# Optimization experiments

Measured on AMD Instinct MI355X. Metric: run time of the kernel, lower is better.

Reference implementation:

```python
import jax, jax.numpy as jnp
import numpy as np

B, C, H, W = 4, 96, 256, 256
WS = 8          # window size
NH = 4          # num heads
SHIFT = 4       # shift size (block_idx=1 -> WS//2)
HD = C // NH    # head dim = 24
N = WS * WS     # tokens per window = 64
MLP_H = 4 * C   # 384
EPS = 1e-6


def _rel_pos_index():
    coords = np.stack(np.meshgrid(np.arange(WS), np.arange(WS), indexing='ij'))  # [2,WS,WS]
    cf = coords.reshape(2, -1)                                                   # [2,N]
    rel = cf[:, :, None] - cf[:, None, :]                                        # [2,N,N]
    rel = rel.transpose(1, 2, 0) + (WS - 1)
    rel[:, :, 0] *= 2 * WS - 1
    return rel.sum(-1)  # [N,N] int


def _attn_mask():
    # standard Swin shifted-window mask, static (numpy)
    img = np.zeros((H, W), dtype=np.float32)
    cnt = 0
    for hs in (slice(0, -WS), slice(-WS, -SHIFT), slice(-SHIFT, None)):
        for ws_ in (slice(0, -WS), slice(-WS, -SHIFT), slice(-SHIFT, None)):
            img[hs, ws_] = cnt
            cnt += 1
    m = img.reshape(H // WS, WS, W // WS, WS).transpose(0, 2, 1, 3).reshape(-1, N)  # [nW,N]
    am = m[:, None, :] - m[:, :, None]
    return np.where(am != 0, -100.0, 0.0).astype(np.float32)  # [nW,N,N]


REL_IDX = _rel_pos_index()
ATTN_MASK = _attn_mask()


def _ln(x, w, b):
    mu = x.mean(-1, keepdims=True)
    var = ((x - mu) ** 2).mean(-1, keepdims=True)
    return (x - mu) * jax.lax.rsqrt(var + EPS) * w + b


def setup_inputs() -> dict:
    key = jax.random.key(0)
    ks = jax.random.split(key, 8)
    s = 0.02
    return {
        'x': jax.random.normal(ks[0], (B, C, H, W), jnp.float32),
        'norm_w': jnp.ones((C,), jnp.float32),
        'norm_b': jnp.zeros((C,), jnp.float32),
        'qkv_w': jax.random.normal(ks[1], (3 * C, C), jnp.float32) * s,
        'qkv_b': jnp.zeros((3 * C,), jnp.float32),
        'proj_w': jax.random.normal(ks[2], (C, C), jnp.float32) * s,
        'proj_b': jnp.zeros((C,), jnp.float32),
        'rpb_table': jax.random.normal(ks[3], ((2 * WS - 1) ** 2, NH), jnp.float32) * s,
        'norm2_w': jnp.ones((C,), jnp.float32),
        'norm2_b': jnp.zeros((C,), jnp.float32),
        'fc1_w': jax.random.normal(ks[4], (MLP_H, C), jnp.float32) * s,
        'fc1_b': jnp.zeros((MLP_H,), jnp.float32),
        'fc2_w': jax.random.normal(ks[5], (C, MLP_H), jnp.float32) * s,
        'fc2_b': jnp.zeros((C,), jnp.float32),
    }


def _swin_msa(y, qkv_w, qkv_b, proj_w, proj_b, rpb_table):
    # y: [B,H,W,C] (already layer-normed)
    ys = jnp.roll(y, shift=(-SHIFT, -SHIFT), axis=(1, 2))
    nWh, nWw = H // WS, W // WS
    # window partition -> [B*nW, N, C]
    xw = ys.reshape(B, nWh, WS, nWw, WS, C).transpose(0, 1, 3, 2, 4, 5).reshape(-1, N, C)
    qkv = xw @ qkv_w.T + qkv_b                       # [Bn,N,3C]
    qkv = qkv.reshape(-1, N, 3, NH, HD).transpose(2, 0, 3, 1, 4)  # [3,Bn,NH,N,HD]
    q, k, v = qkv[0], qkv[1], qkv[2]
    scale = HD ** -0.5
    attn = jnp.einsum('bhnd,bhmd->bhnm', q * scale, k)           # [Bn,NH,N,N]
    bias = rpb_table[jnp.asarray(REL_IDX)].transpose(2, 0, 1)    # [NH,N,N]
    attn = attn + bias[None]
    nW = nWh * nWw
    mask = jnp.asarray(ATTN_MASK)                                # [nW,N,N]
    attn = attn.reshape(B, nW, NH, N, N) + mask[None, :, None]
    attn = jax.nn.softmax(attn.reshape(-1, NH, N, N), axis=-1)
    out = jnp.einsum('bhnm,bhmd->bhnd', attn, v)                 # [Bn,NH,N,HD]
    out = out.transpose(0, 2, 1, 3).reshape(-1, N, C)
    out = out @ proj_w.T + proj_b
    # window reverse
    out = out.reshape(B, nWh, nWw, WS, WS, C).transpose(0, 1, 3, 2, 4, 5).reshape(B, H, W, C)
    return jnp.roll(out, shift=(SHIFT, SHIFT), axis=(1, 2))


def reference(x, norm_w, norm_b, qkv_w, qkv_b, proj_w, proj_b, rpb_table,
              norm2_w, norm2_b, fc1_w, fc1_b, fc2_w, fc2_b):
    xp = x.transpose(0, 2, 3, 1)                                  # [B,H,W,C]
    h = xp + _swin_msa(_ln(xp, norm_w, norm_b), qkv_w, qkv_b, proj_w, proj_b, rpb_table)
    y2 = _ln(h, norm2_w, norm2_b)
    mlp = jax.nn.gelu(y2 @ fc1_w.T + fc1_b, approximate=False) @ fc2_w.T + fc2_b
    h = h + mlp                                                   # proj is Identity (in==out)
    return h.transpose(0, 3, 1, 2)
```

## Files before the change

### kernel.cpp

```cpp
#include <hip/hip_runtime.h>
#include <hip/hip_bf16.h>
#include <math.h>

constexpr int B_    = 4;
constexpr int C_    = 96;
constexpr int H_    = 256;
constexpr int W_    = 256;
constexpr int WS_   = 8;
constexpr int NH_   = 4;
constexpr int SHIFT_= 4;
constexpr int HD_   = 24;
constexpr int NT_   = 64;
constexpr int NWW_  = 32;
constexpr int MLPH_ = 384;
constexpr int HW_   = H_*W_;
constexpr float EPS_   = 1e-6f;
constexpr float SCALE_ = 0.20412414523193150f;

using bf16   = __bf16;
using bf16x8 = __attribute__((ext_vector_type(8))) __bf16;
using bf16x4 = __attribute__((ext_vector_type(4))) __bf16;
using f32x4  = __attribute__((ext_vector_type(4))) float;

__device__ __forceinline__ f32x4 mfma16(bf16x8 a, bf16x8 b, f32x4 c) {
    return __builtin_amdgcn_mfma_f32_16x16x32_bf16(a, b, c, 0, 0, 0);
}

constexpr size_t XT_B    = (size_t)B_*HW_*96*2;
constexpr int    WQ2_E   = 320*96;
constexpr int    WPR_E   = 96*96;
constexpr int    WF1_E   = 384*96;
constexpr int    WF2_E   = 96*384;
constexpr int    WSUM_E  = WQ2_E + WPR_E + WF1_E + WF2_E;
constexpr int    NBQ     = 320;
constexpr int    WBLKS   = (WSUM_E + NBQ + 255)/256;
constexpr int    TBLKS   = B_*HW_/64;

__global__ __launch_bounds__(256) void prep_kernel(
    const float* __restrict__ x,
    const float* __restrict__ qkv_w, const float* __restrict__ qkv_b,
    const float* __restrict__ proj_w, const float* __restrict__ fc1w,
    const float* __restrict__ fc2w,
    bf16* __restrict__ xt, bf16* __restrict__ warena, float* __restrict__ bq2)
{
    __shared__ float st[64*97];
    const int tid = threadIdx.x;
    if (blockIdx.x < WBLKS) {
        int i = blockIdx.x*256 + tid;
        if (i < WQ2_E) {
            int R = i/96, c = i%96;
            int h = R/80, s = R%80;
            float v;
            if      (s < 24) v = qkv_w[(h*24+s)*96 + c] * SCALE_;
            else if (s < 48) v = qkv_w[(96 + h*24 + s-24)*96 + c];
            else if (s < 72) v = qkv_w[(192 + h*24 + s-48)*96 + c];
            else             v = 0.f;
            warena[i] = (bf16)v;
        } else if (i < WQ2_E + WPR_E) {
            warena[i] = (bf16)proj_w[i - WQ2_E];
        } else if (i < WQ2_E + WPR_E + WF1_E) {
            warena[i] = (bf16)fc1w[i - WQ2_E - WPR_E];
        } else if (i < WSUM_E) {
            warena[i] = (bf16)fc2w[i - WQ2_E - WPR_E - WF1_E];
        } else if (i < WSUM_E + NBQ) {
            int j = i - WSUM_E;
            int h = j/80, s = j%80;
            float v;
            if      (s < 24) v = qkv_b[h*24+s] * SCALE_;
            else if (s < 48) v = qkv_b[96 + h*24 + s-24];
            else if (s < 72) v = qkv_b[192 + h*24 + s-48];
            else             v = 0.f;
            bq2[j] = v;
        }
        return;
    }
    const int tb = blockIdx.x - WBLKS;
    const int b  = tb >> 10;
    const int r0 = (tb & 1023)*64;
    const float* xb = x + (size_t)(b*96)*HW_ + r0;
    for (int idx = tid; idx < 6144; idx += 256) {
        int c = idx >> 6, t = idx & 63;
        st[t*97 + c] = xb[(size_t)c*HW_ + t];
    }
    __syncthreads();
    {
        const int t = tid >> 2, qa = tid & 3;
        bf16* dst = xt + ((size_t)(b<<16) + r0 + t)*96 + qa*24;
        const float* sp_ = &st[t*97 + qa*24];
        #pragma unroll
        for (int k = 0; k < 3; ++k) {
            bf16x8 o;
            #pragma unroll
            for (int j = 0; j < 8; ++j) o[j] = (bf16)sp_[k*8 + j];
            *(bf16x8*)(dst + k*8) = o;
        }
    }
}

constexpr int ASQ = 0;
constexpr int ASK = 2560;
constexpr int ASV = 4096;
constexpr int ASP = 5824;
constexpr int AXO = 10432;
constexpr int ASM_N = 17088;

__global__ __launch_bounds__(256) void attn_kernel(
    bf16* __restrict__ xt,
    const float* __restrict__ norm_w, const float* __restrict__ norm_b,
    const bf16*  __restrict__ wq2,
    const float* __restrict__ bq2,
    const bf16*  __restrict__ wproj,
    const float* __restrict__ proj_b,
    const float* __restrict__ rpb)
{
    __shared__ __align__(16) bf16 sm[ASM_N];
    const int tid  = threadIdx.x;
    const int wave = tid >> 6, lane = tid & 63;
    const int l16  = lane & 15, quad = lane >> 4;
    const int blk  = blockIdx.x;
    const int b    = blk >> 10;
    const int wid  = blk & 1023;
    const int wh   = wid >> 5, ww = wid & 31;

    if (tid < 64) { bf16x8 z = {}; *(bf16x8*)&sm[ASQ + tid*40 + 24] = z; }

    const int t  = tid >> 2, qa = tid & 3;
    const int wi = t >> 3, wj = t & 7;
    const int gh = (wh*WS_ + wi + SHIFT_) & (H_-1);
    const int gw = (ww*WS_ + wj + SHIFT_) & (W_-1);
    const size_t pix = (size_t)(b<<16) + gh*W_ + gw;
    {
        const bf16* xp = xt + pix*96 + qa*24;
        float v[24]; float mu = 0.f, ss = 0.f;
        #pragma unroll
        for (int k = 0; k < 3; ++k) {
            bf16x8 h8 = ((const bf16x8*)xp)[k];
            #pragma unroll
            for (int j = 0; j < 8; ++j) {
                v[k*8+j] = (float)h8[j];
                mu += v[k*8+j]; ss += v[k*8+j]*v[k*8+j];
            }
        }
        mu += __shfl_xor(mu,1); mu += __shfl_xor(mu,2);
        ss += __shfl_xor(ss,1); ss += __shfl_xor(ss,2);
        mu *= (1.f/C_);
        float rstd = rsqrtf(ss*(1.f/C_) - mu*mu + EPS_);
        #pragma unroll
        for (int cc = 0; cc < 24; ++cc) {
            int c = qa*24 + cc;
            sm[AXO + t*104 + c] = (bf16)((v[cc]-mu)*rstd*norm_w[c] + norm_b[c]);
        }
    }
    __syncthreads();

    bf16x8 af[4][3];
    #pragma unroll
    for (int mt = 0; mt < 4; ++mt)
        #pragma unroll
        for (int kk = 0; kk < 3; ++kk)
            af[mt][kk] = *(const bf16x8*)&sm[AXO + (mt*16+l16)*104 + kk*32 + quad*8];

    const int qrow0 = wave*16;
    for (int h = 0; h < NH_; ++h) {
        for (int jt = 0; jt < 5; ++jt) {
            if (((h*5 + jt) & 3) != wave) continue;
            const int s   = jt*16 + l16;
            const int row = h*80 + s;
            bf16x8 bw[3];
            #pragma unroll
            for (int kk = 0; kk < 3; ++kk)
                bw[kk] = *(const bf16x8*)(wq2 + (size_t)row*96 + kk*32 + quad*8);
            const float bias = bq2[row];
            #pragma unroll
            for (int mt = 0; mt < 4; ++mt) {
                f32x4 acc = {};
                #pragma unroll
                for (int kk = 0; kk < 3; ++kk) acc = mfma16(af[mt][kk], bw[kk], acc);
                const int tb = mt*16 + quad*4;
                if (s < 24) {
                    #pragma unroll
                    for (int r = 0; r < 4; ++r)
                        sm[ASQ + (tb+r)*40 + s] = (bf16)(acc[r] + bias);
                } else if (s < 48) {
                    #pragma unroll
                    for (int r = 0; r < 4; ++r)
                        sm[ASK + (tb+r)*24 + (s-24)] = (bf16)(acc[r] + bias);
                } else if (s < 72) {
                    bf16x4 pv;
                    #pragma unroll
                    for (int r = 0; r < 4; ++r) pv[r] = (bf16)(acc[r] + bias);
                    *(bf16x4*)&sm[ASV + (s-48)*72 + tb] = pv;
                }
            }
        }
        __syncthreads();

        bf16x8 aq = *(const bf16x8*)&sm[ASQ + (qrow0 + l16)*40 + quad*8];
        f32x4 accS[4];
        #pragma unroll
        for (int kt = 0; kt < 4; ++kt) {
            bf16x8 bk = *(const bf16x8*)&sm[ASK + (kt*16+l16)*24 + quad*8];
            f32x4 z = {};
            accS[kt] = mfma16(aq, bk, z);
        }
        float s_[4][4];
        #pragma unroll
        for (int kt = 0; kt < 4; ++kt) {
            const int key = kt*16 + l16;
            const int ki = key >> 3, kj = key & 7;
            const int labk = (((wh*8+ki) >= H_-WS_) + ((wh*8+ki) >= H_-SHIFT_))*3
                           +  ((ww*8+kj) >= W_-WS_) + ((ww*8+kj) >= W_-SHIFT_);
            #pragma unroll
            for (int r = 0; r < 4; ++r) {
                const int q = qrow0 + quad*4 + r;
                const int ti = q >> 3, tj = q & 7;
                const int labq = (((wh*8+ti) >= H_-WS_) + ((wh*8+ti) >= H_-SHIFT_))*3
                               +  ((ww*8+tj) >= W_-WS_) + ((ww*8+tj) >= W_-SHIFT_);
                const int ridx = (ti - ki + 7)*15 + (tj - kj + 7);
                float val = accS[kt][r] + rpb[ridx*NH_ + h];
                if (labk != labq) val -= 100.f;
                s_[kt][r] = val;
            }
        }
        #pragma unroll
        for (int r = 0; r < 4; ++r) {
            float m = fmaxf(fmaxf(s_[0][r], s_[1][r]), fmaxf(s_[2][r], s_[3][r]));
            m = fmaxf(m, __shfl_xor(m,1)); m = fmaxf(m, __shfl_xor(m,2));
            m = fmaxf(m, __shfl_xor(m,4)); m = fmaxf(m, __shfl_xor(m,8));
            float su = 0.f;
            #pragma unroll
            for (int kt = 0; kt < 4; ++kt) { s_[kt][r] = __expf(s_[kt][r]-m); su += s_[kt][r]; }
            su += __shfl_xor(su,1); su += __shfl_xor(su,2);
            su += __shfl_xor(su,4); su += __shfl_xor(su,8);
            const float inv = 1.f/su;
            #pragma unroll
            for (int kt = 0; kt < 4; ++kt)
                sm[ASP + (qrow0 + quad*4 + r)*72 + kt*16 + l16] = (bf16)(s_[kt][r]*inv);
        }
        __syncthreads();

        bf16x8 ap0 = *(const bf16x8*)&sm[ASP + (qrow0+l16)*72 + quad*8];
        bf16x8 ap1 = *(const bf16x8*)&sm[ASP + (qrow0+l16)*72 + 32 + quad*8];
        #pragma unroll
        for (int nt2 = 0; nt2 < 2; ++nt2) {
            const int d = nt2*16 + l16;
            bf16x8 bv0 = *(const bf16x8*)&sm[ASV + d*72 + quad*8];
            bf16x8 bv1 = *(const bf16x8*)&sm[ASV + d*72 + 32 + quad*8];
            f32x4 acc = {};
            acc = mfma16(ap0, bv0, acc);
            acc = mfma16(ap1, bv1, acc);
            if (d < HD_) {
                #pragma unroll
                for (int r = 0; r < 4; ++r)
                    sm[AXO + (qrow0 + quad*4 + r)*104 + h*24 + d] = (bf16)acc[r];
            }
        }
        __syncthreads();
    }

    {
        bf16x8 ao[3];
        #pragma unroll
        for (int kk = 0; kk < 3; ++kk)
            ao[kk] = *(const bf16x8*)&sm[AXO + (qrow0 + l16)*104 + kk*32 + quad*8];
        for (int nt = 0; nt < 6; ++nt) {
            const int oc = nt*16 + l16;
            bf16x8 bw[3];
            #pragma unroll
            for (int kk = 0; kk < 3; ++kk)
                bw[kk] = *(const bf16x8*)(wproj + (size_t)oc*96 + kk*32 + quad*8);
            f32x4 acc = {};
            #pragma unroll
            for (int kk = 0; kk < 3; ++kk) acc = mfma16(ao[kk], bw[kk], acc);
            #pragma unroll
            for (int r = 0; r < 4; ++r)
                sm[AXO + (qrow0 + quad*4 + r)*104 + oc] = (bf16)acc[r];
        }
    }
    __syncthreads();

    {
        bf16* xp = xt + pix*96 + qa*24;
        #pragma unroll
        for (int k = 0; k < 3; ++k) {
            bf16x8 xv = ((const bf16x8*)xp)[k];
            bf16x8 xo = *(const bf16x8*)&sm[AXO + t*104 + qa*24 + k*8];
            bf16x8 o;
            #pragma unroll
            for (int j = 0; j < 8; ++j)
                o[j] = (bf16)((float)xv[j] + (float)xo[j] + proj_b[qa*24 + k*8 + j]);
            *(bf16x8*)(xp + k*8) = o;
        }
    }
}

constexpr int MSM2  = 8704;

__global__ __launch_bounds__(256) void mlp_kernel(
    const bf16*  __restrict__ hbf,
    const float* __restrict__ n2w, const float* __restrict__ n2b,
    const bf16*  __restrict__ wfc1, const float* __restrict__ fc1b,
    const bf16*  __restrict__ wfc2, const float* __restrict__ fc2b,
    float* __restrict__ out)
{
    __shared__ __align__(16) bf16 sm[MSM2];
    const int tid  = threadIdx.x;
    const int wave = tid >> 6, lane = tid & 63;
    const int l16  = lane & 15, quad = lane >> 4;
    const int pb = blockIdx.x;
    const int b  = pb >> 10;
    const int r0 = (pb & 1023)*64;

    {
        const int t = tid >> 2, qa = tid & 3;
        const bf16* hp = hbf + ((size_t)(b<<16) + r0 + t)*96 + qa*24;
        float v[24]; float mu = 0.f, ss = 0.f;
        #pragma unroll
        for (int k = 0; k < 3; ++k) {
            bf16x8 h8 = ((const bf16x8*)hp)[k];
            #pragma unroll
            for (int j = 0; j < 8; ++j) {
                v[k*8+j] = (float)h8[j];
                mu += v[k*8+j]; ss += v[k*8+j]*v[k*8+j];
            }
        }
        mu += __shfl_xor(mu,1); mu += __shfl_xor(mu,2);
        ss += __shfl_xor(ss,1); ss += __shfl_xor(ss,2);
        mu *= (1.f/C_);
        float rstd = rsqrtf(ss*(1.f/C_) - mu*mu + EPS_);
        #pragma unroll
        for (int k = 0; k < 3; ++k) {
            bf16x8 o;
            #pragma unroll
            for (int j = 0; j < 8; ++j) {
                int c = qa*24 + k*8 + j;
                o[j] = (bf16)((v[k*8+j]-mu)*rstd*n2w[c] + n2b[c]);
            }
            *(bf16x8*)&sm[t*104 + qa*24 + k*8] = o;
        }
    }
    __syncthreads();

    bf16x8 af[4][3];
    #pragma unroll
    for (int mt = 0; mt < 4; ++mt)
        #pragma unroll
        for (int kk = 0; kk < 3; ++kk)
            af[mt][kk] = *(const bf16x8*)&sm[(mt*16+l16)*104 + kk*32 + quad*8];
    __syncthreads();

    f32x4 acc2[6];
    #pragma unroll
    for (int n = 0; n < 6; ++n) acc2[n] = (f32x4){};

    for (int ci = 0; ci < 3; ++ci) {
        #pragma unroll
        for (int rep = 0; rep < 2; ++rep) {
            const int ntl = wave + rep*4;
            const int ub  = ci*128 + ntl*16;
            bf16x8 bw[3];
            #pragma unroll
            for (int kk = 0; kk < 3; ++kk)
                bw[kk] = *(const bf16x8*)(wfc1 + (size_t)(ub + l16)*96 + kk*32 + quad*8);
            const f32x4 b4 = *(const f32x4*)&fc1b[ub + quad*4];
            #pragma unroll
            for (int mt = 0; mt < 4; ++mt) {
                f32x4 acc = {};
                #pragma unroll
                for (int kk = 0; kk < 3; ++kk) acc = mfma16(bw[kk], af[mt][kk], acc);
                bf16x4 g4;
                #pragma unroll
                for (int r = 0; r < 4; ++r) {
                    float tv = acc[r] + b4[r];
                    float u  = tv*tv;
                    float w  = tv*fmaf(-0.0713548165f, u, -1.5957691216f);
                    float e  = __expf(w);
                    g4[r] = (bf16)(tv*__builtin_amdgcn_rcpf(1.f + e));
                }
                *(bf16x4*)&sm[(mt*16 + l16)*136 + ntl*16 + quad*4] = g4;
            }
        }
        __syncthreads();
        bf16x8 ag[4];
        #pragma unroll
        for (int kq = 0; kq < 4; ++kq)
            ag[kq] = *(const bf16x8*)&sm[(wave*16+l16)*136 + kq*32 + quad*8];
        #pragma unroll
        for (int nt2 = 0; nt2 < 6; ++nt2) {
            const int c = nt2*16 + l16;
            #pragma unroll
            for (int kq = 0; kq < 4; ++kq) {
                bf16x8 bw = *(const bf16x8*)(wfc2 + (size_t)c*384 + ci*128 + kq*32 + quad*8);
                acc2[nt2] = mfma16(ag[kq], bw, acc2[nt2]);
            }
        }
        if (ci < 2) __syncthreads();
    }

    {
        const bf16* hres = hbf + ((size_t)(b<<16) + r0)*96;
        float* ob = out + (size_t)(b*96)*HW_ + r0 + wave*16 + quad*4;
        #pragma unroll
        for (int nt2 = 0; nt2 < 6; ++nt2) {
            const int c = nt2*16 + l16;
            const float bias = fc2b[c];
            f32x4 o;
            #pragma unroll
            for (int r = 0; r < 4; ++r) {
                const int row = wave*16 + quad*4 + r;
                o[r] = acc2[nt2][r] + bias + (float)hres[(size_t)row*96 + c];
            }
            *(f32x4*)&ob[(size_t)c*HW_] = o;
        }
    }
}

extern "C" void kernel_launch(void* const* d_in, const int* in_sizes, int n_in,
                              void* d_out, int out_size, void* d_ws, size_t ws_size,
                              hipStream_t stream) {
    const float* x      = (const float*)d_in[0];
    const float* norm_w = (const float*)d_in[1];
    const float* norm_b = (const float*)d_in[2];
    const float* qkv_w  = (const float*)d_in[3];
    const float* qkv_b  = (const float*)d_in[4];
    const float* proj_w = (const float*)d_in[5];
    const float* proj_b = (const float*)d_in[6];
    const float* rpb    = (const float*)d_in[7];
    const float* n2w    = (const float*)d_in[8];
    const float* n2b    = (const float*)d_in[9];
    const float* fc1w   = (const float*)d_in[10];
    const float* fc1b   = (const float*)d_in[11];
    const float* fc2w   = (const float*)d_in[12];
    const float* fc2b   = (const float*)d_in[13];

    float* outp = (float*)d_out;
    char*  ws   = (char*)d_ws;
    bf16*  xt   = (bf16*)ws;
    bf16*  wa   = (bf16*)(ws + XT_B);
    float* bq2  = (float*)(ws + XT_B + (size_t)WSUM_E*2);

    prep_kernel<<<WBLKS + TBLKS, 256, 0, stream>>>(x, qkv_w, qkv_b, proj_w,
                                                   fc1w, fc2w, xt, wa, bq2);
    attn_kernel<<<B_*1024, 256, 0, stream>>>(xt, norm_w, norm_b,
                                             wa, bq2,
                                             wa + WQ2_E, proj_b, rpb);
    mlp_kernel<<<TBLKS, 256, 0, stream>>>(xt, n2w, n2b,
                                          wa + WQ2_E + WPR_E, fc1b,
                                          wa + WQ2_E + WPR_E + WF1_E, fc2b,
                                          outp);
}
```

Before: 532.4 us.

## Fuse input transpose, window attention and MLP into one per-window kernel

The prep, attention and MLP kernels are merged into one kernel per shifted window. It reads the fp32 NCHW input directly with shifted-window gathers, keeps the residual in shared memory and writes the final output straight to the rolled positions. This removes the bf16 NHWC intermediate buffer and its global write and read round trips. Shared memory grows, and a launch bound of 3 blocks per CU constrains register use.

```diff
diff --git a/kernel.cpp b/kernel.cpp
--- a/kernel.cpp
+++ b/kernel.cpp
@@ -10,9 +10,6 @@
 constexpr int NH_   = 4;
 constexpr int SHIFT_= 4;
 constexpr int HD_   = 24;
-constexpr int NT_   = 64;
-constexpr int NWW_  = 32;
-constexpr int MLPH_ = 384;
 constexpr int HW_   = H_*W_;
 constexpr float EPS_   = 1e-6f;
 constexpr float SCALE_ = 0.20412414523193150f;
@@ -26,7 +23,6 @@
     return __builtin_amdgcn_mfma_f32_16x16x32_bf16(a, b, c, 0, 0, 0);
 }
 
-constexpr size_t XT_B    = (size_t)B_*HW_*96*2;
 constexpr int    WQ2_E   = 320*96;
 constexpr int    WPR_E   = 96*96;
 constexpr int    WF1_E   = 384*96;
@@ -34,133 +30,129 @@
 constexpr int    WSUM_E  = WQ2_E + WPR_E + WF1_E + WF2_E;
 constexpr int    NBQ     = 320;
 constexpr int    WBLKS   = (WSUM_E + NBQ + 255)/256;
-constexpr int    TBLKS   = B_*HW_/64;
-
-__global__ __launch_bounds__(256) void prep_kernel(
-    const float* __restrict__ x,
+
+__global__ __launch_bounds__(256) void prepw_kernel(
     const float* __restrict__ qkv_w, const float* __restrict__ qkv_b,
     const float* __restrict__ proj_w, const float* __restrict__ fc1w,
     const float* __restrict__ fc2w,
-    bf16* __restrict__ xt, bf16* __restrict__ warena, float* __restrict__ bq2)
+    bf16* __restrict__ warena, float* __restrict__ bq2)
 {
-    __shared__ float st[64*97];
-    const int tid = threadIdx.x;
-    if (blockIdx.x < WBLKS) {
-        int i = blockIdx.x*256 + tid;
-        if (i < WQ2_E) {
-            int R = i/96, c = i%96;
-            int h = R/80, s = R%80;
-            float v;
-            if      (s < 24) v = qkv_w[(h*24+s)*96 + c] * SCALE_;
-            else if (s < 48) v = qkv_w[(96 + h*24 + s-24)*96 + c];
-            else if (s < 72) v = qkv_w[(192 + h*24 + s-48)*96 + c];
-            else             v = 0.f;
-            warena[i] = (bf16)v;
-        } else if (i < WQ2_E + WPR_E) {
-            warena[i] = (bf16)proj_w[i - WQ2_E];
-        } else if (i < WQ2_E + WPR_E + WF1_E) {
-            warena[i] = (bf16)fc1w[i - WQ2_E - WPR_E];
-        } else if (i < WSUM_E) {
-            warena[i] = (bf16)fc2w[i - WQ2_E - WPR_E - WF1_E];
-        } else if (i < WSUM_E + NBQ) {
-            int j = i - WSUM_E;
-            int h = j/80, s = j%80;
-            float v;
-            if      (s < 24) v = qkv_b[h*24+s] * SCALE_;
-            else if (s < 48) v = qkv_b[96 + h*24 + s-24];
-            else if (s < 72) v = qkv_b[192 + h*24 + s-48];
-            else             v = 0.f;
-            bq2[j] = v;
-        }
-        return;
-    }
-    const int tb = blockIdx.x - WBLKS;
-    const int b  = tb >> 10;
-    const int r0 = (tb & 1023)*64;
-    const float* xb = x + (size_t)(b*96)*HW_ + r0;
-    for (int idx = tid; idx < 6144; idx += 256) {
-        int c = idx >> 6, t = idx & 63;
-        st[t*97 + c] = xb[(size_t)c*HW_ + t];
-    }
-    __syncthreads();
-    {
-        const int t = tid >> 2, qa = tid & 3;
-        bf16* dst = xt + ((size_t)(b<<16) + r0 + t)*96 + qa*24;
-        const float* sp_ = &st[t*97 + qa*24];
-        #pragma unroll
-        for (int k = 0; k < 3; ++k) {
-            bf16x8 o;
-            #pragma unroll
-            for (int j = 0; j < 8; ++j) o[j] = (bf16)sp_[k*8 + j];
-            *(bf16x8*)(dst + k*8) = o;
-        }
+    int i = blockIdx.x*256 + threadIdx.x;
+    if (i < WQ2_E) {
+        int R = i/96, c = i%96;
+        int h = R/80, s = R%80;
+        float v;
+        if      (s < 24) v = qkv_w[(h*24+s)*96 + c] * SCALE_;
+        else if (s < 48) v = qkv_w[(96 + h*24 + s-24)*96 + c];
+        else if (s < 72) v = qkv_w[(192 + h*24 + s-48)*96 + c];
+        else             v = 0.f;
+        warena[i] = (bf16)v;
+    } else if (i < WQ2_E + WPR_E) {
+        warena[i] = (bf16)proj_w[i - WQ2_E];
+    } else if (i < WQ2_E + WPR_E + WF1_E) {
+        warena[i] = (bf16)fc1w[i - WQ2_E - WPR_E];
+    } else if (i < WSUM_E) {
+        warena[i] = (bf16)fc2w[i - WQ2_E - WPR_E - WF1_E];
+    } else if (i < WSUM_E + NBQ) {
+        int j = i - WSUM_E;
+        int h = j/80, s = j%80;
+        float v;
+        if      (s < 24) v = qkv_b[h*24+s] * SCALE_;
+        else if (s < 48) v = qkv_b[96 + h*24 + s-24];
+        else if (s < 72) v = qkv_b[192 + h*24 + s-48];
+        else             v = 0.f;
+        bq2[j] = v;
     }
 }
 
-constexpr int ASQ = 0;
-constexpr int ASK = 2560;
-constexpr int ASV = 4096;
-constexpr int ASP = 5824;
-constexpr int AXO = 10432;
-constexpr int ASM_N = 17088;
-
-__global__ __launch_bounds__(256) void attn_kernel(
-    bf16* __restrict__ xt,
+constexpr int XR_E  = 0;
+constexpr int AXO_E = 6656;
+constexpr int SCR_E = 13312;
+constexpr int ASQ_E = SCR_E;
+constexpr int ASK_E = SCR_E + 2560;
+constexpr int ASV_E = SCR_E + 4096;
+constexpr int ASP_E = SCR_E + 5824;
+constexpr int MYG_E = SCR_E;
+constexpr int SM_E  = SCR_E + 12416;
+
+__global__ __launch_bounds__(256, 3) void fused_kernel(
+    const float* __restrict__ x,
     const float* __restrict__ norm_w, const float* __restrict__ norm_b,
     const bf16*  __restrict__ wq2,
     const float* __restrict__ bq2,
     const bf16*  __restrict__ wproj,
     const float* __restrict__ proj_b,
-    const float* __restrict__ rpb)
+    const float* __restrict__ rpb,
+    const float* __restrict__ n2w, const float* __restrict__ n2b,
+    const bf16*  __restrict__ wfc1, const float* __restrict__ fc1b,
+    const bf16*  __restrict__ wfc2, const float* __restrict__ fc2b,
+    float* __restrict__ out)
 {
-    __shared__ __align__(16) bf16 sm[ASM_N];
+    __shared__ __align__(16) bf16 sm[SM_E];
+    float* stage = (float*)&sm[SCR_E];
+
     const int tid  = threadIdx.x;
     const int wave = tid >> 6, lane = tid & 63;
     const int l16  = lane & 15, quad = lane >> 4;
-    const int blk  = blockIdx.x;
-    const int b    = blk >> 10;
-    const int wid  = blk & 1023;
-    const int wh   = wid >> 5, ww = wid & 31;
-
-    if (tid < 64) { bf16x8 z = {}; *(bf16x8*)&sm[ASQ + tid*40 + 24] = z; }
-
     const int t  = tid >> 2, qa = tid & 3;
-    const int wi = t >> 3, wj = t & 7;
-    const int gh = (wh*WS_ + wi + SHIFT_) & (H_-1);
-    const int gw = (ww*WS_ + wj + SHIFT_) & (W_-1);
-    const size_t pix = (size_t)(b<<16) + gh*W_ + gw;
+    const int qrow0 = wave*16;
+
+    const int blk = blockIdx.x;
+    const int b   = blk >> 10;
+    const int wid = blk & 1023;
+    const int wh  = wid >> 5, ww = wid & 31;
+
+    #pragma unroll
+    for (int it = 0; it < 6; ++it) {
+        const int i2  = it*256 + tid;
+        const int c   = i2 >> 4;
+        const int rem = i2 & 15;
+        const int wi  = rem >> 1;
+        const int wj4 = (rem & 1)*4;
+        const int gh  = (wh*WS_ + wi + SHIFT_) & (H_-1);
+        const int gw0 = (ww*WS_ + wj4 + SHIFT_) & (W_-1);
+        f32x4 v4 = *(const f32x4*)(x + (size_t)(b*96 + c)*HW_ + gh*W_ + gw0);
+        #pragma unroll
+        for (int j = 0; j < 4; ++j)
+            stage[(wi*8 + wj4 + j)*97 + c] = v4[j];
+    }
+    __syncthreads();
+
     {
-        const bf16* xp = xt + pix*96 + qa*24;
         float v[24]; float mu = 0.f, ss = 0.f;
         #pragma unroll
-        for (int k = 0; k < 3; ++k) {
-            bf16x8 h8 = ((const bf16x8*)xp)[k];
-            #pragma unroll
-            for (int j = 0; j < 8; ++j) {
-                v[k*8+j] = (float)h8[j];
-                mu += v[k*8+j]; ss += v[k*8+j]*v[k*8+j];
-            }
+        for (int cc = 0; cc < 24; ++cc) {
+            v[cc] = stage[t*97 + qa*24 + cc];
+            mu += v[cc]; ss += v[cc]*v[cc];
         }
         mu += __shfl_xor(mu,1); mu += __shfl_xor(mu,2);
         ss += __shfl_xor(ss,1); ss += __shfl_xor(ss,2);
         mu *= (1.f/C_);
         float rstd = rsqrtf(ss*(1.f/C_) - mu*mu + EPS_);
         #pragma unroll
-        for (int cc = 0; cc < 24; ++cc) {
-            int c = qa*24 + cc;
-            sm[AXO + t*104 + c] = (bf16)((v[cc]-mu)*rstd*norm_w[c] + norm_b[c]);
+        for (int k = 0; k < 3; ++k) {
+            bf16x8 xv8, ln8;
+            #pragma unroll
+            for (int j = 0; j < 8; ++j) {
+                const int c = qa*24 + k*8 + j;
+                xv8[j] = (bf16)v[k*8+j];
+                ln8[j] = (bf16)((v[k*8+j]-mu)*rstd*norm_w[c] + norm_b[c]);
+            }
+            *(bf16x8*)&sm[XR_E  + t*104 + qa*24 + k*8] = xv8;
+            *(bf16x8*)&sm[AXO_E + t*104 + qa*24 + k*8] = ln8;
         }
     }
     __syncthreads();
+
+    if (tid < 64) { bf16x8 z = {}; *(bf16x8*)&sm[ASQ_E + tid*40 + 24] = z; }
 
     bf16x8 af[4][3];
     #pragma unroll
     for (int mt = 0; mt < 4; ++mt)
         #pragma unroll
         for (int kk = 0; kk < 3; ++kk)
-            af[mt][kk] = *(const bf16x8*)&sm[AXO + (mt*16+l16)*104 + kk*32 + quad*8];
-
-    const int qrow0 = wave*16;
+            af[mt][kk] = *(const bf16x8*)&sm[AXO_E + (mt*16+l16)*104 + kk*32 + quad*8];
+
     for (int h = 0; h < NH_; ++h) {
         for (int jt = 0; jt < 5; ++jt) {
             if (((h*5 + jt) & 3) != wave) continue;
@@ -180,26 +172,26 @@
                 if (s < 24) {
                     #pragma unroll
                     for (int r = 0; r < 4; ++r)
-                        sm[ASQ + (tb+r)*40 + s] = (bf16)(acc[r] + bias);
+                        sm[ASQ_E + (tb+r)*40 + s] = (bf16)(acc[r] + bias);
                 } else if (s < 48) {
                     #pragma unroll
                     for (int r = 0; r < 4; ++r)
-                        sm[ASK + (tb+r)*24 + (s-24)] = (bf16)(acc[r] + bias);
+                        sm[ASK_E + (tb+r)*24 + (s-24)] = (bf16)(acc[r] + bias);
                 } else if (s < 72) {
                     bf16x4 pv;
                     #pragma unroll
                     for (int r = 0; r < 4; ++r) pv[r] = (bf16)(acc[r] + bias);
-                    *(bf16x4*)&sm[ASV + (s-48)*72 + tb] = pv;
+                    *(bf16x4*)&sm[ASV_E + (s-48)*72 + tb] = pv;
                 }
             }
         }
         __syncthreads();
 
-        bf16x8 aq = *(const bf16x8*)&sm[ASQ + (qrow0 + l16)*40 + quad*8];
+        bf16x8 aq = *(const bf16x8*)&sm[ASQ_E + (qrow0 + l16)*40 + quad*8];
         f32x4 accS[4];
         #pragma unroll
         for (int kt = 0; kt < 4; ++kt) {
-            bf16x8 bk = *(const bf16x8*)&sm[ASK + (kt*16+l16)*24 + quad*8];
+            bf16x8 bk = *(const bf16x8*)&sm[ASK_E + (kt*16+l16)*24 + quad*8];
             f32x4 z = {};
             accS[kt] = mfma16(aq, bk, z);
         }
@@ -235,24 +227,24 @@
             const float inv = 1.f/su;
             #pragma unroll
             for (int kt = 0; kt < 4; ++kt)
-                sm[ASP + (qrow0 + quad*4 + r)*72 + kt*16 + l16] = (bf16)(s_[kt][r]*inv);
+                sm[ASP_E + (qrow0 + quad*4 + r)*72 + kt*16 + l16] = (bf16)(s_[kt][r]*inv);
         }
         __syncthreads();
 
-        bf16x8 ap0 = *(const bf16x8*)&sm[ASP + (qrow0+l16)*72 + quad*8];
-        bf16x8 ap1 = *(const bf16x8*)&sm[ASP + (qrow0+l16)*72 + 32 + quad*8];
+        bf16x8 ap0 = *(const bf16x8*)&sm[ASP_E + (qrow0+l16)*72 + quad*8];
+        bf16x8 ap1 = *(const bf16x8*)&sm[ASP_E + (qrow0+l16)*72 + 32 + quad*8];
         #pragma unroll
         for (int nt2 = 0; nt2 < 2; ++nt2) {
             const int d = nt2*16 + l16;
-            bf16x8 bv0 = *(const bf16x8*)&sm[ASV + d*72 + quad*8];
-            bf16x8 bv1 = *(const bf16x8*)&sm[ASV + d*72 + 32 + quad*8];
+            bf16x8 bv0 = *(const bf16x8*)&sm[ASV_E + d*72 + quad*8];
+            bf16x8 bv1 = *(const bf16x8*)&sm[ASV_E + d*72 + 32 + quad*8];
             f32x4 acc = {};
             acc = mfma16(ap0, bv0, acc);
             acc = mfma16(ap1, bv1, acc);
             if (d < HD_) {
                 #pragma unroll
                 for (int r = 0; r < 4; ++r)
-                    sm[AXO + (qrow0 + quad*4 + r)*104 + h*24 + d] = (bf16)acc[r];
+                    sm[AXO_E + (qrow0 + quad*4 + r)*104 + h*24 + d] = (bf16)acc[r];
             }
         }
         __syncthreads();
@@ -262,7 +254,7 @@
         bf16x8 ao[3];
         #pragma unroll
         for (int kk = 0; kk < 3; ++kk)
-            ao[kk] = *(const bf16x8*)&sm[AXO + (qrow0 + l16)*104 + kk*32 + quad*8];
+            ao[kk] = *(const bf16x8*)&sm[AXO_E + (qrow0 + l16)*104 + kk*32 + quad*8];
         for (int nt = 0; nt < 6; ++nt) {
             const int oc = nt*16 + l16;
             bf16x8 bw[3];
@@ -274,55 +266,27 @@
             for (int kk = 0; kk < 3; ++kk) acc = mfma16(ao[kk], bw[kk], acc);
             #pragma unroll
             for (int r = 0; r < 4; ++r)
-                sm[AXO + (qrow0 + quad*4 + r)*104 + oc] = (bf16)acc[r];
+                sm[AXO_E + (qrow0 + quad*4 + r)*104 + oc] = (bf16)acc[r];
         }
     }
     __syncthreads();
 
     {
-        bf16* xp = xt + pix*96 + qa*24;
+        float hv[24]; float mu = 0.f, ss = 0.f;
         #pragma unroll
         for (int k = 0; k < 3; ++k) {
-            bf16x8 xv = ((const bf16x8*)xp)[k];
-            bf16x8 xo = *(const bf16x8*)&sm[AXO + t*104 + qa*24 + k*8];
-            bf16x8 o;
-            #pragma unroll
-            for (int j = 0; j < 8; ++j)
-                o[j] = (bf16)((float)xv[j] + (float)xo[j] + proj_b[qa*24 + k*8 + j]);
-            *(bf16x8*)(xp + k*8) = o;
-        }
-    }
-}
-
-constexpr int MSM2  = 8704;
-
-__global__ __launch_bounds__(256) void mlp_kernel(
-    const bf16*  __restrict__ hbf,
-    const float* __restrict__ n2w, const float* __restrict__ n2b,
-    const bf16*  __restrict__ wfc1, const float* __restrict__ fc1b,
-    const bf16*  __restrict__ wfc2, const float* __restrict__ fc2b,
-    float* __restrict__ out)
-{
-    __shared__ __align__(16) bf16 sm[MSM2];
-    const int tid  = threadIdx.x;
-    const int wave = tid >> 6, lane = tid & 63;
-    const int l16  = lane & 15, quad = lane >> 4;
-    const int pb = blockIdx.x;
-    const int b  = pb >> 10;
-    const int r0 = (pb & 1023)*64;
-
-    {
-        const int t = tid >> 2, qa = tid & 3;
-        const bf16* hp = hbf + ((size_t)(b<<16) + r0 + t)*96 + qa*24;
-        float v[24]; float mu = 0.f, ss = 0.f;
-        #pragma unroll
-        for (int k = 0; k < 3; ++k) {
-            bf16x8 h8 = ((const bf16x8*)hp)[k];
+            bf16x8 xv = *(const bf16x8*)&sm[XR_E  + t*104 + qa*24 + k*8];
+            bf16x8 po = *(const bf16x8*)&sm[AXO_E + t*104 + qa*24 + k*8];
+            bf16x8 h8;
             #pragma unroll
             for (int j = 0; j < 8; ++j) {
-                v[k*8+j] = (float)h8[j];
-                mu += v[k*8+j]; ss += v[k*8+j]*v[k*8+j];
-            }
+                float hf = (float)xv[j] + (float)po[j] + proj_b[qa*24 + k*8 + j];
+                h8[j] = (bf16)hf;
+                float hb = (float)h8[j];
+                hv[k*8+j] = hb;
+                mu += hb; ss += hb*hb;
+            }
+            *(bf16x8*)&sm[XR_E + t*104 + qa*24 + k*8] = h8;
         }
         mu += __shfl_xor(mu,1); mu += __shfl_xor(mu,2);
         ss += __shfl_xor(ss,1); ss += __shfl_xor(ss,2);
@@ -333,20 +297,20 @@
             bf16x8 o;
             #pragma unroll
             for (int j = 0; j < 8; ++j) {
-                int c = qa*24 + k*8 + j;
-                o[j] = (bf16)((v[k*8+j]-mu)*rstd*n2w[c] + n2b[c]);
-            }
-            *(bf16x8*)&sm[t*104 + qa*24 + k*8] = o;
+                const int c = qa*24 + k*8 + j;
+                o[j] = (bf16)((hv[k*8+j]-mu)*rstd*n2w[c] + n2b[c]);
+            }
+            *(bf16x8*)&sm[MYG_E + t*104 + qa*24 + k*8] = o;
         }
     }
     __syncthreads();
 
-    bf16x8 af[4][3];
+    bf16x8 af2[4][3];
     #pragma unroll
     for (int mt = 0; mt < 4; ++mt)
         #pragma unroll
         for (int kk = 0; kk < 3; ++kk)
-            af[mt][kk] = *(const bf16x8*)&sm[(mt*16+l16)*104 + kk*32 + quad*8];
+            af2[mt][kk] = *(const bf16x8*)&sm[MYG_E + (mt*16+l16)*104 + kk*32 + quad*8];
     __syncthreads();
 
     f32x4 acc2[6];
@@ -367,24 +331,24 @@
             for (int mt = 0; mt < 4; ++mt) {
                 f32x4 acc = {};
                 #pragma unroll
-                for (int kk = 0; kk < 3; ++kk) acc = mfma16(bw[kk], af[mt][kk], acc);
+                for (int kk = 0; kk < 3; ++kk) acc = mfma16(bw[kk], af2[mt][kk], acc);
                 bf16x4 g4;
                 #pragma unroll
                 for (int r = 0; r < 4; ++r) {
                     float tv = acc[r] + b4[r];
-                    float u  = tv*tv;
-                    float w  = tv*fmaf(-0.0713548165f, u, -1.5957691216f);
+                    float uu = tv*tv;
+                    float w  = tv*fmaf(-0.0713548165f, uu, -1.5957691216f);
                     float e  = __expf(w);
                     g4[r] = (bf16)(tv*__builtin_amdgcn_rcpf(1.f + e));
                 }
-                *(bf16x4*)&sm[(mt*16 + l16)*136 + ntl*16 + quad*4] = g4;
+                *(bf16x4*)&sm[MYG_E + (mt*16 + l16)*136 + ntl*16 + quad*4] = g4;
             }
         }
         __syncthreads();
         bf16x8 ag[4];
         #pragma unroll
         for (int kq = 0; kq < 4; ++kq)
-            ag[kq] = *(const bf16x8*)&sm[(wave*16+l16)*136 + kq*32 + quad*8];
+            ag[kq] = *(const bf16x8*)&sm[MYG_E + (wave*16+l16)*136 + kq*32 + quad*8];
         #pragma unroll
         for (int nt2 = 0; nt2 < 6; ++nt2) {
             const int c = nt2*16 + l16;
@@ -398,19 +362,18 @@
     }
 
     {
-        const bf16* hres = hbf + ((size_t)(b<<16) + r0)*96;
-        float* ob = out + (size_t)(b*96)*HW_ + r0 + wave*16 + quad*4;
+        const int row = wave*16 + quad*4;
+        const int gh  = (wh*WS_ + (row>>3) + SHIFT_) & (H_-1);
+        const int gw0 = (ww*WS_ + (row&7)  + SHIFT_) & (W_-1);
         #pragma unroll
         for (int nt2 = 0; nt2 < 6; ++nt2) {
             const int c = nt2*16 + l16;
             const float bias = fc2b[c];
             f32x4 o;
             #pragma unroll
-            for (int r = 0; r < 4; ++r) {
-                const int row = wave*16 + quad*4 + r;
-                o[r] = acc2[nt2][r] + bias + (float)hres[(size_t)row*96 + c];
-            }
-            *(f32x4*)&ob[(size_t)c*HW_] = o;
+            for (int r = 0; r < 4; ++r)
+                o[r] = acc2[nt2][r] + bias + (float)sm[XR_E + (row+r)*104 + c];
+            *(f32x4*)(out + (size_t)(b*96 + c)*HW_ + gh*W_ + gw0) = o;
         }
     }
 }
@@ -435,17 +398,15 @@
 
     float* outp = (float*)d_out;
     char*  ws   = (char*)d_ws;
-    bf16*  xt   = (bf16*)ws;
-    bf16*  wa   = (bf16*)(ws + XT_B);
-    float* bq2  = (float*)(ws + XT_B + (size_t)WSUM_E*2);
-
-    prep_kernel<<<WBLKS + TBLKS, 256, 0, stream>>>(x, qkv_w, qkv_b, proj_w,
-                                                   fc1w, fc2w, xt, wa, bq2);
-    attn_kernel<<<B_*1024, 256, 0, stream>>>(xt, norm_w, norm_b,
-                                             wa, bq2,
-                                             wa + WQ2_E, proj_b, rpb);
-    mlp_kernel<<<TBLKS, 256, 0, stream>>>(xt, n2w, n2b,
-                                          wa + WQ2_E + WPR_E, fc1b,
-                                          wa + WQ2_E + WPR_E + WF1_E, fc2b,
-                                          outp);
+    bf16*  wa   = (bf16*)ws;
+    float* bq2  = (float*)(ws + (size_t)WSUM_E*2);
+
+    prepw_kernel<<<WBLKS, 256, 0, stream>>>(qkv_w, qkv_b, proj_w, fc1w, fc2w, wa, bq2);
+    fused_kernel<<<B_*1024, 256, 0, stream>>>(x, norm_w, norm_b,
+                                              wa, bq2,
+                                              wa + WQ2_E, proj_b, rpb,
+                                              n2w, n2b,
+                                              wa + WQ2_E + WPR_E, fc1b,
+                                              wa + WQ2_E + WPR_E + WF1_E, fc2b,
+                                              outp);
 }
```

Result: no change. 523.6 us (-1.7%).
